# Kernel optimization log

Measured on AMD Instinct MI355X. Metric: run time of the kernel, lower is better.

Reference implementation:

```python
import jax, jax.numpy as jnp
import numpy as np

E = 768
NH_REG = 6   # num_heads - cultural_heads
NH_CUL = 2   # cultural_heads


def _branch(x, wq, bq, wk, bk, wv, bv, wo, bo, cb, nh, mask_add):
    # x: [B,T,E]; weights stored as [in,out]; cb: [1,nh,1,hd]
    B, T, Edim = x.shape
    hd = Edim // nh
    scale = hd ** -0.5
    q = (x @ wq + bq).reshape(B, T, nh, hd).transpose(0, 2, 1, 3)
    k = (x @ wk + bk).reshape(B, T, nh, hd).transpose(0, 2, 1, 3)
    v = (x @ wv + bv).reshape(B, T, nh, hd).transpose(0, 2, 1, 3)
    q = q + cb  # learned cultural bias added to Q
    scores = jnp.einsum('bhtd,bhsd->bhts', q, k) * scale
    scores = scores + mask_add
    w = jax.nn.softmax(scores, axis=-1)  # dropout omitted (eval mode)
    out = jnp.einsum('bhts,bhsd->bhtd', w, v)
    out = out.transpose(0, 2, 1, 3).reshape(B, T, Edim)
    return out @ wo + bo


def setup_inputs() -> dict:
    key = jax.random.key(0)
    ks = jax.random.split(key, 24)
    B, S = 2, 2048
    d = {
        'hidden_states': jax.random.normal(ks[0], (B, S, E), jnp.float32),
        'cultural_mask': jax.random.normal(ks[1], (B, S, S), jnp.float32),
        'attention_mask': jax.random.normal(ks[2], (B, 1, 1, S), jnp.float32),
    }
    s = E ** -0.5
    names = ['rq_w', 'rk_w', 'rv_w', 'ro_w', 'cq_w', 'ck_w', 'cv_w', 'co_w']
    for i, n in enumerate(names):
        d[n] = jax.random.normal(ks[3 + i], (E, E), jnp.float32) * s
    for i, n in enumerate(['rq_b', 'rk_b', 'rv_b', 'ro_b', 'cq_b', 'ck_b', 'cv_b', 'co_b']):
        d[n] = jax.random.normal(ks[11 + i], (E,), jnp.float32) * 0.02
    d['r_cb'] = jnp.zeros((1, NH_REG, 1, E // NH_REG), jnp.float32)
    d['c_cb'] = jnp.zeros((1, NH_CUL, 1, E // NH_CUL), jnp.float32)
    # NOTE: concat of two branches gives 2E features -> out layer maps 2E -> E
    d['out_w'] = jax.random.normal(ks[19], (2 * E, E), jnp.float32) * (2 * E) ** -0.5
    d['out_b'] = jax.random.normal(ks[20], (E,), jnp.float32) * 0.02
    return d


def reference(hidden_states, cultural_mask, attention_mask,
              rq_w, rk_w, rv_w, ro_w, cq_w, ck_w, cv_w, co_w,
              rq_b, rk_b, rv_b, ro_b, cq_b, ck_b, cv_b, co_b,
              r_cb, c_cb, out_w, out_b):
    # regular branch: attention_mask only
    reg = _branch(hidden_states, rq_w, rq_b, rk_w, rk_b, rv_w, rv_b,
                  ro_w, ro_b, r_cb, NH_REG, attention_mask)
    # cultural branch: cultural_mask (broadcast over heads) + attention_mask
    cmask = cultural_mask[:, None, :, :] + attention_mask
    cul = _branch(hidden_states, cq_w, cq_b, ck_w, ck_b, cv_w, cv_b,
                  co_w, co_b, c_cb, NH_CUL, cmask)
    combined = jnp.concatenate([reg, cul], axis=-1)  # [B,T,2E]
    return combined @ out_w + out_b
```

## Files before the change

### kernel.cpp

```cpp
#include <hip/hip_runtime.h>
#include <hip/hip_bf16.h>

using u16 = unsigned short;
using u32 = unsigned int;
typedef short short8 __attribute__((ext_vector_type(8)));
typedef float f32x4 __attribute__((ext_vector_type(4)));

#define B_  2
#define S_  2048
#define E_  768
#define BS_ 4096

#define L2E_ 1.44269504088896f
#define FML2_ 17.3123404906676f

__device__ __forceinline__ u16 f2bf(float f) {
  __hip_bfloat16 h = __float2bfloat16(f);
  return *reinterpret_cast<u16*>(&h);
}

__device__ __forceinline__ u32 pk2(float a, float b) {
  return (u32)f2bf(a) | ((u32)f2bf(b) << 16);
}

__device__ __forceinline__ void gld16(const void* g, void* l) {
  __builtin_amdgcn_global_load_lds(
      (const __attribute__((address_space(1))) u32*)g,
      (__attribute__((address_space(3))) u32*)l, 16, 0, 0);
}


__global__ __launch_bounds__(256) void conv_x_k(const float* __restrict__ x,
                                                u16* __restrict__ xb, int n4) {
  int i = blockIdx.x * 256 + threadIdx.x;
  if (i >= n4) return;
  float4 v = reinterpret_cast<const float4*>(x)[i];
  reinterpret_cast<uint2*>(xb)[i] = make_uint2(pk2(v.x, v.y), pk2(v.z, v.w));
}

__global__ __launch_bounds__(256) void bias_k(
    const float* rqb, const float* rkb, const float* rvb,
    const float* cqb, const float* ckb, const float* cvb,
    const float* rob, const float* cob,
    const float* rcb, const float* ccb,
    float* bqkv, float* bproj) {
  int t = blockIdx.x * 256 + threadIdx.x;
  if (t < 4608) {
    int seg = t / 768, i = t - seg * 768;
    float v = 0.f;
    if      (seg == 0) v = rqb[i] + rcb[i];
    else if (seg == 1) v = rkb[i];
    else if (seg == 2) v = rvb[i];
    else if (seg == 3) v = cqb[i] + ccb[i];
    else if (seg == 4) v = ckb[i];
    else               v = cvb[i];
    bqkv[t] = v;
  } else {
    int u = t - 4608;
    if (u < 1536) bproj[u] = (u < 768) ? rob[u] : cob[u - 768];
  }
}

struct TP {
  const float* src[9];
  u16* dst[9];
  int rows[9];
};

__global__ __launch_bounds__(256) void transpose_k(TP p) {
  int mi = blockIdx.z;
  int rows = p.rows[mi];
  int r0 = blockIdx.y * 32;
  if (r0 >= rows) return;
  int c0 = blockIdx.x * 32;
  const float* src = p.src[mi];
  u16* dst = p.dst[mi];
  __shared__ float t[32][33];
  int tx = threadIdx.x & 31, ty = threadIdx.x >> 5;
#pragma unroll
  for (int d = 0; d < 4; ++d) {
    int r = ty + d * 8;
    t[r][tx] = src[(size_t)(r0 + r) * 768 + c0 + tx];
  }
  __syncthreads();
#pragma unroll
  for (int d = 0; d < 4; ++d) {
    int c = ty + d * 8;
    dst[(size_t)(c0 + c) * rows + r0 + tx] = f2bf(t[tx][c]);
  }
}


template<int MODE>
__global__ __launch_bounds__(256) void gemm_t_k(
    const u16* __restrict__ A, int lda,
    const u16* __restrict__ BT, int ldb,
    const float* __restrict__ bias, int K,
    const u16* __restrict__ A2, int msplit, int bofs,
    void* __restrict__ Cout, int ldc,
    u16* __restrict__ Qr, u16* __restrict__ Kr, u16* __restrict__ Vtr,
    u16* __restrict__ Qc, u16* __restrict__ Kc, u16* __restrict__ Vtc) {
  __shared__ u16 lA[128 * 32];
  __shared__ u16 lB[128 * 32];
  const int tid = threadIdx.x, w = tid >> 6, lane = tid & 63;
  const int quad = lane >> 4, l15 = lane & 15;
  const int m0 = blockIdx.y * 128, n0 = blockIdx.x * 128;
  if (msplit && m0 >= msplit) { A = A2 - (size_t)msplit * lda; BT += bofs; }

  const f32x4 z4 = {0.f, 0.f, 0.f, 0.f};
  f32x4 acc[4][4];
#pragma unroll
  for (int i = 0; i < 4; ++i)
#pragma unroll
    for (int j = 0; j < 4; ++j) acc[i][j] = z4;

  const int sr = w * 32 + (lane >> 2);
  const int scp = lane & 3;

  for (int kt = 0; kt < K; kt += 32) {
    int r1 = sr, r2 = sr + 16;
    int c1 = (scp - (r1 >> 2)) & 3;
    int c2 = (scp - (r2 >> 2)) & 3;
    gld16(A + (size_t)(m0 + r1) * lda + kt + c1 * 8, &lA[r1 * 32 + scp * 8]);
    gld16(A + (size_t)(m0 + r2) * lda + kt + c2 * 8, &lA[r2 * 32 + scp * 8]);
    gld16(BT + (size_t)(n0 + r1) * ldb + kt + c1 * 8, &lB[r1 * 32 + scp * 8]);
    gld16(BT + (size_t)(n0 + r2) * ldb + kt + c2 * 8, &lB[r2 * 32 + scp * 8]);
    __syncthreads();
    short8 af[4], bg[4];
#pragma unroll
    for (int i = 0; i < 4; ++i) {
      int r = (w >> 1) * 64 + i * 16 + l15;
      af[i] = *reinterpret_cast<const short8*>(&lA[r * 32 + ((quad + (r >> 2)) & 3) * 8]);
    }
#pragma unroll
    for (int j = 0; j < 4; ++j) {
      int r = (w & 1) * 64 + j * 16 + l15;
      bg[j] = *reinterpret_cast<const short8*>(&lB[r * 32 + ((quad + (r >> 2)) & 3) * 8]);
    }
#pragma unroll
    for (int i = 0; i < 4; ++i)
#pragma unroll
      for (int j = 0; j < 4; ++j)
        acc[i][j] = __builtin_amdgcn_mfma_f32_16x16x32_bf16(af[i], bg[j], acc[i][j], 0, 0, 0);
    __syncthreads();
  }

  const int seg = (MODE == 2) ? (m0 / 768) : 0;
#pragma unroll
  for (int i = 0; i < 4; ++i) {
    int f = m0 + (w >> 1) * 64 + i * 16 + quad * 4;
    float4 b4 = *reinterpret_cast<const float4*>(bias + f);
#pragma unroll
    for (int j = 0; j < 4; ++j) {
      int t = n0 + (w & 1) * 64 + j * 16 + l15;
      float v0 = acc[i][j][0] + b4.x;
      float v1 = acc[i][j][1] + b4.y;
      float v2 = acc[i][j][2] + b4.z;
      float v3 = acc[i][j][3] + b4.w;
      if (MODE == 0) {
        *reinterpret_cast<uint2*>((u16*)Cout + (size_t)t * ldc + f) =
            make_uint2(pk2(v0, v1), pk2(v2, v3));
      } else if (MODE == 1) {
        *reinterpret_cast<float4*>((float*)Cout + (size_t)t * ldc + f) =
            make_float4(v0, v1, v2, v3);
      } else {
        int b = t >> 11, s = t & 2047;
        int fs = f - seg * 768;
        if (seg == 0) {
          int h = fs >> 7, d = fs & 127;
          *reinterpret_cast<uint2*>(Qr + ((size_t)(b * 6 + h) * 2048 + s) * 128 + d) =
              make_uint2(pk2(v0, v1), pk2(v2, v3));
        } else if (seg == 1) {
          int h = fs >> 7, d = fs & 127;
          *reinterpret_cast<uint2*>(Kr + ((size_t)(b * 6 + h) * 2048 + s) * 128 + d) =
              make_uint2(pk2(v0, v1), pk2(v2, v3));
        } else if (seg == 2) {
          int h = fs >> 7, d = fs & 127;
          u16* vp = Vtr + ((size_t)(b * 6 + h) * 128 + d) * 2048 + s;
          vp[0] = f2bf(v0); vp[2048] = f2bf(v1); vp[4096] = f2bf(v2); vp[6144] = f2bf(v3);
        } else if (seg == 3) {
          int h = fs / 384, d = fs - h * 384;
          *reinterpret_cast<uint2*>(Qc + ((size_t)(b * 2 + h) * 2048 + s) * 384 + d) =
              make_uint2(pk2(v0, v1), pk2(v2, v3));
        } else if (seg == 4) {
          int h = fs / 384, d = fs - h * 384;
          *reinterpret_cast<uint2*>(Kc + ((size_t)(b * 2 + h) * 2048 + s) * 384 + d) =
              make_uint2(pk2(v0, v1), pk2(v2, v3));
        } else {
          int h = fs / 384, d = fs - h * 384;
          u16* vp = Vtc + ((size_t)(b * 2 + h) * 384 + d) * 2048 + s;
          vp[0] = f2bf(v0); vp[2048] = f2bf(v1); vp[4096] = f2bf(v2); vp[6144] = f2bf(v3);
        }
      }
    }
  }
}

__global__ __launch_bounds__(256) void attn_g1_k(
    const u16* __restrict__ Qr, const u16* __restrict__ Kr,
    const u16* __restrict__ Qc, const u16* __restrict__ Kc,
    u16* __restrict__ Pr, u16* __restrict__ Pc, float* __restrict__ Lp,
    const float* __restrict__ am, const float* __restrict__ cmask,
    float sReg, float sCul, int zoff) {
  __shared__ u16 lA[128 * 32];
  __shared__ u16 lB[128 * 32];
  const int tid = threadIdx.x, w = tid >> 6, lane = tid & 63;
  const int quad = lane >> 4, l15 = lane & 15;
  const int m0 = blockIdx.y * 128, n0 = blockIdx.x * 128;
  const int gz = zoff + blockIdx.z;
  const u16 *A, *BT;
  u16* P;
  const float* cm = nullptr;
  float scl;
  int K, b;
  if (gz < 12) {
    A = Kr + (size_t)gz * S_ * 128;
    BT = Qr + (size_t)gz * S_ * 128;
    K = 128;
    P = Pr + (size_t)blockIdx.z * (size_t)S_ * S_;
    scl = sReg;
    b = gz / 6;
  } else {
    int hc = gz - 12;
    A = Kc + (size_t)hc * S_ * 384;
    BT = Qc + (size_t)hc * S_ * 384;
    K = 384;
    P = Pc + (size_t)hc * (size_t)S_ * S_;
    b = hc >> 1;
    cm = cmask + (size_t)b * S_ * S_;
    scl = sCul;
  }

  const f32x4 z4 = {0.f, 0.f, 0.f, 0.f};
  f32x4 acc[4][4];
#pragma unroll
  for (int i = 0; i < 4; ++i)
#pragma unroll
    for (int j = 0; j < 4; ++j) acc[i][j] = z4;

  const int sr = w * 32 + (lane >> 2);
  const int scp = lane & 3;

  for (int kt = 0; kt < K; kt += 32) {
    int r1 = sr, r2 = sr + 16;
    int c1 = (scp - (r1 >> 2)) & 3;
    int c2 = (scp - (r2 >> 2)) & 3;
    gld16(A + (size_t)(m0 + r1) * K + kt + c1 * 8, &lA[r1 * 32 + scp * 8]);
    gld16(A + (size_t)(m0 + r2) * K + kt + c2 * 8, &lA[r2 * 32 + scp * 8]);
    gld16(BT + (size_t)(n0 + r1) * K + kt + c1 * 8, &lB[r1 * 32 + scp * 8]);
    gld16(BT + (size_t)(n0 + r2) * K + kt + c2 * 8, &lB[r2 * 32 + scp * 8]);
    __syncthreads();
    short8 af[4], bg[4];
#pragma unroll
    for (int i = 0; i < 4; ++i) {
      int r = (w >> 1) * 64 + i * 16 + l15;
      af[i] = *reinterpret_cast<const short8*>(&lA[r * 32 + ((quad + (r >> 2)) & 3) * 8]);
    }
#pragma unroll
    for (int j = 0; j < 4; ++j) {
      int r = (w & 1) * 64 + j * 16 + l15;
      bg[j] = *reinterpret_cast<const short8*>(&lB[r * 32 + ((quad + (r >> 2)) & 3) * 8]);
    }
#pragma unroll
    for (int i = 0; i < 4; ++i)
#pragma unroll
      for (int j = 0; j < 4; ++j)
        acc[i][j] = __builtin_amdgcn_mfma_f32_16x16x32_bf16(af[i], bg[j], acc[i][j], 0, 0, 0);
    __syncthreads();
  }

  const float* amb = am + b * S_;
  float lsum[4] = {0.f, 0.f, 0.f, 0.f};
#pragma unroll
  for (int i = 0; i < 4; ++i) {
    int kb = m0 + (w >> 1) * 64 + i * 16 + quad * 4;
    float4 a4 = *reinterpret_cast<const float4*>(amb + kb);
    float pre0 = fmaf(a4.x, L2E_, -FML2_);
    float pre1 = fmaf(a4.y, L2E_, -FML2_);
    float pre2 = fmaf(a4.z, L2E_, -FML2_);
    float pre3 = fmaf(a4.w, L2E_, -FML2_);
#pragma unroll
    for (int j = 0; j < 4; ++j) {
      int q = n0 + (w & 1) * 64 + j * 16 + l15;
      float c0 = pre0, c1 = pre1, c2 = pre2, c3 = pre3;
      if (cm) {
        float4 cmv = *reinterpret_cast<const float4*>(cm + (size_t)q * S_ + kb);
        c0 = fmaf(cmv.x, L2E_, c0);
        c1 = fmaf(cmv.y, L2E_, c1);
        c2 = fmaf(cmv.z, L2E_, c2);
        c3 = fmaf(cmv.w, L2E_, c3);
      }
      float p0 = exp2f(fmaf(acc[i][j][0], scl, c0));
      float p1 = exp2f(fmaf(acc[i][j][1], scl, c1));
      float p2 = exp2f(fmaf(acc[i][j][2], scl, c2));
      float p3 = exp2f(fmaf(acc[i][j][3], scl, c3));
      lsum[j] += (p0 + p1) + (p2 + p3);
      *reinterpret_cast<uint2*>(P + (size_t)q * S_ + kb) =
          make_uint2(pk2(p0, p1), pk2(p2, p3));
    }
  }
#pragma unroll
  for (int j = 0; j < 4; ++j) {
    float s = lsum[j];
    s += __shfl_xor(s, 16);
    s += __shfl_xor(s, 32);
    if (lane < 16)
      Lp[(size_t)gz * (32 * S_) + ((size_t)((m0 >> 7) * 2 + (w >> 1))) * S_ +
         n0 + (w & 1) * 64 + j * 16 + lane] = s;
  }
}

__global__ __launch_bounds__(256) void attn_g2_k(
    const u16* __restrict__ Pr, const u16* __restrict__ Pc,
    const u16* __restrict__ Vtr, const u16* __restrict__ Vtc,
    const float* __restrict__ Lp, u16* __restrict__ AO, int zoff) {
  const int gz = zoff + blockIdx.z;
  const int m0 = blockIdx.y * 128, n0 = blockIdx.x * 128;
  const u16 *A, *BT;
  int b, colbase;
  if (gz < 12) {
    if (blockIdx.y) return;
    A = Vtr + (size_t)gz * 128 * S_;
    BT = Pr + (size_t)blockIdx.z * (size_t)S_ * S_;
    b = gz / 6;
    colbase = (gz % 6) * 128;
  } else {
    int hc = gz - 12;
    A = Vtc + (size_t)hc * 384 * S_;
    BT = Pc + (size_t)hc * (size_t)S_ * S_;
    b = hc >> 1;
    colbase = 768 + (hc & 1) * 384;
  }
  __shared__ u16 lA[128 * 32];
  __shared__ u16 lB[128 * 32];
  __shared__ float lL[128];
  const int tid = threadIdx.x, w = tid >> 6, lane = tid & 63;
  const int quad = lane >> 4, l15 = lane & 15;

  if (tid < 128) {
    const float* lp = Lp + (size_t)gz * (32 * S_) + (n0 + tid);
    float s = 0.f;
#pragma unroll
    for (int g = 0; g < 32; ++g) s += lp[(size_t)g * S_];
    lL[tid] = 1.f / s;
  }

  const f32x4 z4 = {0.f, 0.f, 0.f, 0.f};
  f32x4 acc[4][4];
#pragma unroll
  for (int i = 0; i < 4; ++i)
#pragma unroll
    for (int j = 0; j < 4; ++j) acc[i][j] = z4;

  const int sr = w * 32 + (lane >> 2);
  const int scp = lane & 3;

  for (int kt = 0; kt < S_; kt += 32) {
    int r1 = sr, r2 = sr + 16;
    int c1 = (scp - (r1 >> 2)) & 3;
    int c2 = (scp - (r2 >> 2)) & 3;
    gld16(A + (size_t)(m0 + r1) * S_ + kt + c1 * 8, &lA[r1 * 32 + scp * 8]);
    gld16(A + (size_t)(m0 + r2) * S_ + kt + c2 * 8, &lA[r2 * 32 + scp * 8]);
    gld16(BT + (size_t)(n0 + r1) * S_ + kt + c1 * 8, &lB[r1 * 32 + scp * 8]);
    gld16(BT + (size_t)(n0 + r2) * S_ + kt + c2 * 8, &lB[r2 * 32 + scp * 8]);
    __syncthreads();
    short8 af[4], bg[4];
#pragma unroll
    for (int i = 0; i < 4; ++i) {
      int r = (w >> 1) * 64 + i * 16 + l15;
      af[i] = *reinterpret_cast<const short8*>(&lA[r * 32 + ((quad + (r >> 2)) & 3) * 8]);
    }
#pragma unroll
    for (int j = 0; j < 4; ++j) {
      int r = (w & 1) * 64 + j * 16 + l15;
      bg[j] = *reinterpret_cast<const short8*>(&lB[r * 32 + ((quad + (r >> 2)) & 3) * 8]);
    }
#pragma unroll
    for (int i = 0; i < 4; ++i)
#pragma unroll
      for (int j = 0; j < 4; ++j)
        acc[i][j] = __builtin_amdgcn_mfma_f32_16x16x32_bf16(af[i], bg[j], acc[i][j], 0, 0, 0);
    __syncthreads();
  }

  float invl[4];
#pragma unroll
  for (int j = 0; j < 4; ++j) invl[j] = lL[(w & 1) * 64 + j * 16 + l15];
#pragma unroll
  for (int i = 0; i < 4; ++i) {
    int feat = colbase + m0 + (w >> 1) * 64 + i * 16 + quad * 4;
#pragma unroll
    for (int j = 0; j < 4; ++j) {
      int q = n0 + (w & 1) * 64 + j * 16 + l15;
      float v0 = acc[i][j][0] * invl[j];
      float v1 = acc[i][j][1] * invl[j];
      float v2 = acc[i][j][2] * invl[j];
      float v3 = acc[i][j][3] * invl[j];
      *reinterpret_cast<uint2*>(AO + ((size_t)(b * S_ + q)) * 1536 + feat) =
          make_uint2(pk2(v0, v1), pk2(v2, v3));
    }
  }
}


extern "C" void kernel_launch(void* const* d_in, const int* in_sizes, int n_in,
                              void* d_out, int out_size, void* d_ws, size_t ws_size,
                              hipStream_t stream) {
  const float* x     = (const float*)d_in[0];
  const float* cmask = (const float*)d_in[1];
  const float* amask = (const float*)d_in[2];
  const float* W[8]  = { (const float*)d_in[3], (const float*)d_in[4], (const float*)d_in[5],
                         (const float*)d_in[6], (const float*)d_in[7], (const float*)d_in[8],
                         (const float*)d_in[9], (const float*)d_in[10] };
  const float* rq_b = (const float*)d_in[11];
  const float* rk_b = (const float*)d_in[12];
  const float* rv_b = (const float*)d_in[13];
  const float* ro_b = (const float*)d_in[14];
  const float* cq_b = (const float*)d_in[15];
  const float* ck_b = (const float*)d_in[16];
  const float* cv_b = (const float*)d_in[17];
  const float* co_b = (const float*)d_in[18];
  const float* r_cb = (const float*)d_in[19];
  const float* c_cb = (const float*)d_in[20];
  const float* out_w = (const float*)d_in[21];
  const float* out_b = (const float*)d_in[22];

  char* p = (char*)d_ws;
  auto carve = [&](size_t bytes) -> void* {
    void* r = (void*)p;
    p += (bytes + 255) & ~(size_t)255;
    return r;
  };
  u16* Xb    = (u16*)carve((size_t)BS_ * E_ * 2);
  u16* WqkvT = (u16*)carve((size_t)4608 * 768 * 2);
  u16* roT   = (u16*)carve((size_t)768 * 768 * 2);
  u16* coT   = (u16*)carve((size_t)768 * 768 * 2);
  u16* outwT = (u16*)carve((size_t)768 * 1536 * 2);
  float* bqkv  = (float*)carve(4608 * 4);
  float* bproj = (float*)carve(1536 * 4);
  u16* Qr  = (u16*)carve((size_t)B_ * 6 * S_ * 128 * 2);
  u16* Kr  = (u16*)carve((size_t)B_ * 6 * S_ * 128 * 2);
  u16* Vtr = (u16*)carve((size_t)B_ * 6 * S_ * 128 * 2);
  u16* Qc  = (u16*)carve((size_t)B_ * 2 * S_ * 384 * 2);
  u16* Kc  = (u16*)carve((size_t)B_ * 2 * S_ * 384 * 2);
  u16* Vtc = (u16*)carve((size_t)B_ * 2 * S_ * 384 * 2);
  u16* AO  = (u16*)carve((size_t)BS_ * 1536 * 2);

  float* Lp = (float*)Xb;
  u16* Pcul = (u16*)carve((size_t)4 * S_ * S_ * 2);
  size_t used = (size_t)(p - (char*)d_ws);
  size_t rem = (ws_size > used) ? (ws_size - used) : 0;
  int RCH;
  if      (rem >= (size_t)12 * S_ * S_ * 2 + 4096) RCH = 12;
  else if (rem >= (size_t)4  * S_ * S_ * 2 + 4096) RCH = 4;
  else                                             RCH = 2;
  u16* Preg = (u16*)carve((size_t)RCH * S_ * S_ * 2);
  u16* PR = Pcul;

  const float sReg = 0.08838834764831845f * L2E_;
  const float sCul = 0.05103103630798288f * L2E_;

  conv_x_k<<<dim3(BS_ * E_ / 4 / 256), 256, 0, stream>>>(x, Xb, BS_ * E_ / 4);
  bias_k<<<dim3(24), 256, 0, stream>>>(rq_b, rk_b, rv_b, cq_b, ck_b, cv_b,
                                       ro_b, co_b, r_cb, c_cb, bqkv, bproj);

  TP tp;
  const int wsel[6] = {0, 1, 2, 4, 5, 6};
  for (int i = 0; i < 6; ++i) {
    tp.src[i] = W[wsel[i]];
    tp.dst[i] = WqkvT + (size_t)i * 768 * 768;
    tp.rows[i] = 768;
  }
  tp.src[6] = W[3]; tp.dst[6] = roT;   tp.rows[6] = 768;
  tp.src[7] = W[7]; tp.dst[7] = coT;   tp.rows[7] = 768;
  tp.src[8] = out_w; tp.dst[8] = outwT; tp.rows[8] = 1536;
  transpose_k<<<dim3(24, 48, 9), 256, 0, stream>>>(tp);

  gemm_t_k<2><<<dim3(32, 36), 256, 0, stream>>>(
      WqkvT, 768, Xb, 768, bqkv, 768,
      (const u16*)nullptr, 0, 0, (void*)nullptr, 0,
      Qr, Kr, Vtr, Qc, Kc, Vtc);

  if (RCH == 12) {
    attn_g1_k<<<dim3(16, 16, 16), 256, 0, stream>>>(
        Qr, Kr, Qc, Kc, Preg, Pcul, Lp, amask, cmask, sReg, sCul, 0);
    attn_g2_k<<<dim3(16, 3, 16), 256, 0, stream>>>(
        Preg, Pcul, Vtr, Vtc, Lp, AO, 0);
  } else {
    attn_g1_k<<<dim3(16, 16, 4), 256, 0, stream>>>(
        Qr, Kr, Qc, Kc, Preg, Pcul, Lp, amask, cmask, sReg, sCul, 12);
    attn_g2_k<<<dim3(16, 3, 4), 256, 0, stream>>>(
        Preg, Pcul, Vtr, Vtc, Lp, AO, 12);
    for (int c = 0; c < 12; c += RCH) {
      attn_g1_k<<<dim3(16, 16, RCH), 256, 0, stream>>>(
          Qr, Kr, Qc, Kc, Preg, Pcul, Lp, amask, cmask, sReg, sCul, c);
      attn_g2_k<<<dim3(16, 1, RCH), 256, 0, stream>>>(
          Preg, Pcul, Vtr, Vtc, Lp, AO, c);
    }
  }

  gemm_t_k<0><<<dim3(32, 12), 256, 0, stream>>>(
      roT, 768, AO, 1536, bproj, 768,
      coT, 768, 768, (void*)PR, 1536,
      nullptr, nullptr, nullptr, nullptr, nullptr, nullptr);

  gemm_t_k<1><<<dim3(32, 6), 256, 0, stream>>>(
      outwT, 1536, PR, 1536, out_b, 1536,
      (const u16*)nullptr, 0, 0, d_out, 768,
      nullptr, nullptr, nullptr, nullptr, nullptr, nullptr);
}
```

Baseline: 403.1 us.

## Fuse regular-branch attention into a single flash-style kernel without materialized probabilities

Adds a fused attention kernel for the six regular heads that computes QK^T, the masked exponent and P·V per 64-query tile, keeping probabilities in shared memory instead of writing a full S×S bf16 P matrix to global memory. The softmax uses a fixed max offset (FML2_) rather than a running max, so it does no rescaling and normalizes by the accumulated row sum at the end. The cultural heads still use the two-pass materialized path. This removes large global P traffic and the chunking logic, at the cost of relying on the fixed offset for numerical range and a grid of only 384 blocks.

```diff
diff --git a/kernel.cpp b/kernel.cpp
--- a/kernel.cpp
+++ b/kernel.cpp
@@ -196,6 +196,168 @@
   }
 }
 
+__global__ __launch_bounds__(256) void attn_freg_k(
+    const u16* __restrict__ Qr, const u16* __restrict__ Kr,
+    const u16* __restrict__ Vtr, const float* __restrict__ am,
+    u16* __restrict__ AO, float scl) {
+  __shared__ u16 lQ[64 * 128];
+  __shared__ u16 lK[128 * 32];
+  __shared__ u16 lV[128 * 32];
+  __shared__ u16 lP[64 * 128];
+  __shared__ float lL[2][64];
+
+  const int tid = threadIdx.x, w = tid >> 6, lane = tid & 63;
+  const int quad = lane >> 4, l15 = lane & 15;
+  const int L = blockIdx.x;
+  const int gg = (L & 7) * 48 + (L >> 3);
+  const int bh = gg >> 5;
+  const int q0 = (gg & 31) * 64;
+  const int b = bh / 6, h = bh - b * 6;
+
+  const u16* Qb = Qr + ((size_t)bh * S_ + q0) * 128;
+  const u16* Kb0 = Kr + (size_t)bh * S_ * 128;
+  const u16* Vb0 = Vtr + (size_t)bh * 128 * S_;
+  const float* amb = am + b * S_;
+
+#pragma unroll
+  for (int it = 0; it < 4; ++it) {
+    int idx = it * 256 + tid;
+    int row = idx >> 4, gs = idx & 15;
+    gld16(Qb + (size_t)row * 128 + (size_t)(gs ^ (row & 15)) * 8, &lQ[idx * 8]);
+  }
+
+  const f32x4 z4 = {0.f, 0.f, 0.f, 0.f};
+  f32x4 accO[4][2];
+#pragma unroll
+  for (int i = 0; i < 4; ++i)
+#pragma unroll
+    for (int j = 0; j < 2; ++j) accO[i][j] = z4;
+  float lsum[2] = {0.f, 0.f};
+
+  const int sr = w * 32 + (lane >> 2);
+  const int scp = lane & 3;
+  const int r1 = sr, r2 = sr + 16;
+  const int c1 = (scp - (r1 >> 2)) & 3;
+  const int c2 = (scp - (r2 >> 2)) & 3;
+  const int khalf = w >> 1, qhalf = w & 1;
+
+  for (int t = 0; t < 16; ++t) {
+    const u16* Kb = Kb0 + (size_t)(t * 128) * 128;
+    f32x4 accS[4][2];
+#pragma unroll
+    for (int i = 0; i < 4; ++i)
+#pragma unroll
+      for (int j = 0; j < 2; ++j) accS[i][j] = z4;
+
+#pragma unroll
+    for (int c = 0; c < 4; ++c) {
+      gld16(Kb + (size_t)r1 * 128 + c * 32 + c1 * 8, &lK[r1 * 32 + scp * 8]);
+      gld16(Kb + (size_t)r2 * 128 + c * 32 + c2 * 8, &lK[r2 * 32 + scp * 8]);
+      __syncthreads();
+      short8 af[4], bg[2];
+#pragma unroll
+      for (int i = 0; i < 4; ++i) {
+        int r = khalf * 64 + i * 16 + l15;
+        af[i] = *reinterpret_cast<const short8*>(&lK[r * 32 + ((quad + (r >> 2)) & 3) * 8]);
+      }
+#pragma unroll
+      for (int j = 0; j < 2; ++j) {
+        int q = qhalf * 32 + j * 16 + l15;
+        int s = (4 * c + quad) ^ (q & 15);
+        bg[j] = *reinterpret_cast<const short8*>(&lQ[q * 128 + s * 8]);
+      }
+#pragma unroll
+      for (int i = 0; i < 4; ++i)
+#pragma unroll
+        for (int j = 0; j < 2; ++j)
+          accS[i][j] = __builtin_amdgcn_mfma_f32_16x16x32_bf16(af[i], bg[j], accS[i][j], 0, 0, 0);
+      __syncthreads();
+    }
+
+#pragma unroll
+    for (int i = 0; i < 4; ++i) {
+      int kb = khalf * 64 + i * 16 + quad * 4;
+      float4 a4 = *reinterpret_cast<const float4*>(amb + t * 128 + kb);
+      float p0c = fmaf(a4.x, L2E_, -FML2_);
+      float p1c = fmaf(a4.y, L2E_, -FML2_);
+      float p2c = fmaf(a4.z, L2E_, -FML2_);
+      float p3c = fmaf(a4.w, L2E_, -FML2_);
+      int sg = (kb >> 3) ^ 0;
+      int so = kb & 7;
+#pragma unroll
+      for (int j = 0; j < 2; ++j) {
+        int q = qhalf * 32 + j * 16 + l15;
+        float p0 = exp2f(fmaf(accS[i][j][0], scl, p0c));
+        float p1 = exp2f(fmaf(accS[i][j][1], scl, p1c));
+        float p2 = exp2f(fmaf(accS[i][j][2], scl, p2c));
+        float p3 = exp2f(fmaf(accS[i][j][3], scl, p3c));
+        lsum[j] += (p0 + p1) + (p2 + p3);
+        int s = ((kb >> 3) ^ (q & 15));
+        *reinterpret_cast<uint2*>(&lP[q * 128 + s * 8 + so]) =
+            make_uint2(pk2(p0, p1), pk2(p2, p3));
+      }
+      (void)sg;
+    }
+    __syncthreads();
+
+    const u16* Vb = Vb0 + t * 128;
+#pragma unroll
+    for (int c = 0; c < 4; ++c) {
+      gld16(Vb + (size_t)r1 * S_ + c * 32 + c1 * 8, &lV[r1 * 32 + scp * 8]);
+      gld16(Vb + (size_t)r2 * S_ + c * 32 + c2 * 8, &lV[r2 * 32 + scp * 8]);
+      __syncthreads();
+      short8 af[4], bg[2];
+#pragma unroll
+      for (int i = 0; i < 4; ++i) {
+        int r = khalf * 64 + i * 16 + l15;
+        af[i] = *reinterpret_cast<const short8*>(&lV[r * 32 + ((quad + (r >> 2)) & 3) * 8]);
+      }
+#pragma unroll
+      for (int j = 0; j < 2; ++j) {
+        int q = qhalf * 32 + j * 16 + l15;
+        int s = (4 * c + quad) ^ (q & 15);
+        bg[j] = *reinterpret_cast<const short8*>(&lP[q * 128 + s * 8]);
+      }
+#pragma unroll
+      for (int i = 0; i < 4; ++i)
+#pragma unroll
+        for (int j = 0; j < 2; ++j)
+          accO[i][j] = __builtin_amdgcn_mfma_f32_16x16x32_bf16(af[i], bg[j], accO[i][j], 0, 0, 0);
+      __syncthreads();
+    }
+  }
+
+#pragma unroll
+  for (int j = 0; j < 2; ++j) {
+    float s = lsum[j];
+    s += __shfl_xor(s, 16);
+    s += __shfl_xor(s, 32);
+    if (lane < 16) lL[khalf][qhalf * 32 + j * 16 + lane] = s;
+  }
+  __syncthreads();
+
+  float invl[2];
+#pragma unroll
+  for (int j = 0; j < 2; ++j) {
+    int q = qhalf * 32 + j * 16 + l15;
+    invl[j] = 1.f / (lL[0][q] + lL[1][q]);
+  }
+#pragma unroll
+  for (int i = 0; i < 4; ++i) {
+    int d = khalf * 64 + i * 16 + quad * 4;
+#pragma unroll
+    for (int j = 0; j < 2; ++j) {
+      int tok = q0 + qhalf * 32 + j * 16 + l15;
+      float v0 = accO[i][j][0] * invl[j];
+      float v1 = accO[i][j][1] * invl[j];
+      float v2 = accO[i][j][2] * invl[j];
+      float v3 = accO[i][j][3] * invl[j];
+      *reinterpret_cast<uint2*>(AO + ((size_t)(b * S_ + tok)) * 1536 + h * 128 + d) =
+          make_uint2(pk2(v0, v1), pk2(v2, v3));
+    }
+  }
+}
+
 __global__ __launch_bounds__(256) void attn_g1_k(
     const u16* __restrict__ Qr, const u16* __restrict__ Kr,
     const u16* __restrict__ Qc, const u16* __restrict__ Kc,
@@ -448,13 +610,6 @@
 
   float* Lp = (float*)Xb;
   u16* Pcul = (u16*)carve((size_t)4 * S_ * S_ * 2);
-  size_t used = (size_t)(p - (char*)d_ws);
-  size_t rem = (ws_size > used) ? (ws_size - used) : 0;
-  int RCH;
-  if      (rem >= (size_t)12 * S_ * S_ * 2 + 4096) RCH = 12;
-  else if (rem >= (size_t)4  * S_ * S_ * 2 + 4096) RCH = 4;
-  else                                             RCH = 2;
-  u16* Preg = (u16*)carve((size_t)RCH * S_ * S_ * 2);
   u16* PR = Pcul;
 
   const float sReg = 0.08838834764831845f * L2E_;
@@ -481,23 +636,12 @@
       (const u16*)nullptr, 0, 0, (void*)nullptr, 0,
       Qr, Kr, Vtr, Qc, Kc, Vtc);
 
-  if (RCH == 12) {
-    attn_g1_k<<<dim3(16, 16, 16), 256, 0, stream>>>(
-        Qr, Kr, Qc, Kc, Preg, Pcul, Lp, amask, cmask, sReg, sCul, 0);
-    attn_g2_k<<<dim3(16, 3, 16), 256, 0, stream>>>(
-        Preg, Pcul, Vtr, Vtc, Lp, AO, 0);
-  } else {
-    attn_g1_k<<<dim3(16, 16, 4), 256, 0, stream>>>(
-        Qr, Kr, Qc, Kc, Preg, Pcul, Lp, amask, cmask, sReg, sCul, 12);
-    attn_g2_k<<<dim3(16, 3, 4), 256, 0, stream>>>(
-        Preg, Pcul, Vtr, Vtc, Lp, AO, 12);
-    for (int c = 0; c < 12; c += RCH) {
-      attn_g1_k<<<dim3(16, 16, RCH), 256, 0, stream>>>(
-          Qr, Kr, Qc, Kc, Preg, Pcul, Lp, amask, cmask, sReg, sCul, c);
-      attn_g2_k<<<dim3(16, 1, RCH), 256, 0, stream>>>(
-          Preg, Pcul, Vtr, Vtc, Lp, AO, c);
-    }
-  }
+  attn_freg_k<<<dim3(384), 256, 0, stream>>>(Qr, Kr, Vtr, amask, AO, sReg);
+
+  attn_g1_k<<<dim3(16, 16, 4), 256, 0, stream>>>(
+      Qr, Kr, Qc, Kc, (u16*)nullptr, Pcul, Lp, amask, cmask, sReg, sCul, 12);
+  attn_g2_k<<<dim3(16, 3, 4), 256, 0, stream>>>(
+      (const u16*)nullptr, Pcul, Vtr, Vtc, Lp, AO, 12);
 
   gemm_t_k<0><<<dim3(32, 12), 256, 0, stream>>>(
       roT, 768, AO, 1536, bproj, 768,
```

Result: slower. 426.7 us (+5.9%).
